# Optimization experiments

Hardware: AMD Instinct MI355X
Metric: run time of the kernel (lower is better)

## Reference

```python
import jax, jax.numpy as jnp
import numpy as np

D = 2048
H = 16
HD = D // H  # 128


def setup_inputs() -> dict:
    key = jax.random.key(0)
    k1, k2, k3 = jax.random.split(key, 3)
    x = jax.random.normal(k1, (2, 2048, D), dtype=jnp.float32)
    # nn.Linear(d, 3d, bias=False): weight [3d, d]; y = x @ W.T
    w_qkv = jax.random.normal(k2, (3 * D, D), dtype=jnp.float32) * (1.0 / np.sqrt(D))
    w_o = jax.random.normal(k3, (D, D), dtype=jnp.float32) * (1.0 / np.sqrt(D))
    return {"x": x, "w_qkv": w_qkv, "w_o": w_o}


def reference(x, w_qkv, w_o):
    B, T, _ = x.shape
    qkv = jnp.einsum('btd,ed->bte', x, w_qkv)  # [B,T,3D]
    q, k, v = jnp.split(qkv, 3, axis=-1)
    # [B,T,D] -> [B,H,T,hd]
    q = q.reshape(B, T, H, HD).transpose(0, 2, 1, 3)
    k = k.reshape(B, T, H, HD).transpose(0, 2, 1, 3)
    v = v.reshape(B, T, H, HD).transpose(0, 2, 1, 3)
    att = jnp.einsum('bhtd,bhsd->bhts', q, k) / np.sqrt(HD).astype(np.float32)
    att = jax.nn.softmax(att, axis=-1)
    y = jnp.einsum('bhts,bhsd->bhtd', att, v)
    y = y.transpose(0, 2, 1, 3).reshape(B, T, D)
    return jnp.einsum('btd,ed->bte', y, w_o)
```

## Files before the change

### kernel.cpp

```cpp
#include <hip/hip_runtime.h>
#include <hip/hip_bf16.h>
#include <math.h>

typedef __bf16 bf16_t;
typedef __attribute__((ext_vector_type(8))) __bf16 bx8;
typedef __attribute__((ext_vector_type(4))) __bf16 bx4;
typedef __attribute__((ext_vector_type(4))) float fx4;

#define DEV __device__ __forceinline__

DEV void async_copy16(void* lds, const void* g) {
    __builtin_amdgcn_global_load_lds(
        (const __attribute__((address_space(1))) unsigned int*)g,
        (__attribute__((address_space(3))) unsigned int*)lds, 16, 0, 0);
}

__global__ void __launch_bounds__(256) cvt_bf16(const float* __restrict__ in,
                                                bf16_t* __restrict__ out, int n) {
    int i = (blockIdx.x * 256 + threadIdx.x) * 4;
    if (i + 3 < n) {
        float4 v = *(const float4*)(in + i);
        bx4 o = { (__bf16)v.x, (__bf16)v.y, (__bf16)v.z, (__bf16)v.w };
        *(bx4*)(out + i) = o;
    }
}

template <bool BF16_OUT>
__global__ void __launch_bounds__(256, 2) gemm_bt(const bf16_t* __restrict__ A,
                                                  const bf16_t* __restrict__ B,
                                                  void* __restrict__ C,
                                                  int M, int N, int K) {
    __shared__ bf16_t As[2 * 4096];
    __shared__ bf16_t Bs[2 * 4096];
    const int tid = threadIdx.x;
    const int w = tid >> 6, lane = tid & 63;
    const int ln = lane & 15, quad = lane >> 4;
    const int m0 = blockIdx.y * 128, n0 = blockIdx.x * 128;
    const int wm = (w >> 1) * 64, wn = (w & 1) * 64;

    fx4 acc[4][4];
#pragma unroll
    for (int i = 0; i < 4; ++i)
#pragma unroll
        for (int j = 0; j < 4; ++j) acc[i][j] = (fx4){0.f, 0.f, 0.f, 0.f};

    for (int k0 = 0; k0 < K; k0 += 64) {
#pragma unroll
        for (int call = 0; call < 4; ++call) {
            int c = w * 256 + call * 64 + lane;
            int p = c >> 9, row = (c >> 2) & 127, piece = c & 3;
            async_copy16(As + (size_t)(w * 256 + call * 64) * 8,
                         A + (size_t)(m0 + row) * K + k0 + p * 32 + piece * 8);
            async_copy16(Bs + (size_t)(w * 256 + call * 64) * 8,
                         B + (size_t)(n0 + row) * K + k0 + p * 32 + piece * 8);
        }
        __syncthreads();

#pragma unroll
        for (int kk = 0; kk < 2; ++kk) {
            bx8 af[4], bf[4];
#pragma unroll
            for (int i = 0; i < 4; ++i)
                af[i] = *(const bx8*)(As + (size_t)kk * 4096 + (wm + i * 16 + ln) * 32 + quad * 8);
#pragma unroll
            for (int j = 0; j < 4; ++j)
                bf[j] = *(const bx8*)(Bs + (size_t)kk * 4096 + (wn + j * 16 + ln) * 32 + quad * 8);
#pragma unroll
            for (int i = 0; i < 4; ++i)
#pragma unroll
                for (int j = 0; j < 4; ++j)
                    acc[i][j] = __builtin_amdgcn_mfma_f32_16x16x32_bf16(af[i], bf[j], acc[i][j], 0, 0, 0);
        }
        __syncthreads();
    }

#pragma unroll
    for (int i = 0; i < 4; ++i) {
        int mrow = m0 + wm + i * 16 + quad * 4;
#pragma unroll
        for (int j = 0; j < 4; ++j) {
            int ncol = n0 + wn + j * 16 + ln;
#pragma unroll
            for (int r = 0; r < 4; ++r) {
                if (BF16_OUT)
                    ((bf16_t*)C)[(size_t)(mrow + r) * N + ncol] = (__bf16)acc[i][j][r];
                else
                    ((float*)C)[(size_t)(mrow + r) * N + ncol] = acc[i][j][r];
            }
        }
    }
}

__global__ void __launch_bounds__(256) vtrans(const bf16_t* __restrict__ qkv,
                                              bf16_t* __restrict__ vt) {
    __shared__ bf16_t tile[64][65];
    const int tid = threadIdx.x;
    const int bh = blockIdx.z;
    const int b = bh >> 4, h = bh & 15;
    const int t0 = blockIdx.x * 64, hd0 = blockIdx.y * 64;
    const bf16_t* src = qkv + (size_t)(b * 2048 + t0) * 6144 + 4096 + h * 128 + hd0;
    const int rr = tid >> 6, cc = tid & 63;
#pragma unroll
    for (int i = 0; i < 16; ++i)
        tile[rr + i * 4][cc] = src[(size_t)(rr + i * 4) * 6144 + cc];
    __syncthreads();
    bf16_t* dst = vt + ((size_t)bh * 128 + hd0) * 2048 + t0;
#pragma unroll
    for (int i = 0; i < 16; ++i)
        dst[(size_t)(rr + i * 4) * 2048 + cc] = tile[cc][rr + i * 4];
}

__global__ void __launch_bounds__(256, 2) attn(const bf16_t* __restrict__ qkv,
                                               const bf16_t* __restrict__ vt,
                                               bf16_t* __restrict__ y) {
    __shared__ bf16_t Ks[128 * 128];
    __shared__ bf16_t Vs[128 * 128];
    __shared__ bf16_t Ps[4 * 1024];
    const int tid = threadIdx.x;
    const int w = tid >> 6, lane = tid & 63;
    const int ln = lane & 15, quad = lane >> 4;
    const int lin = blockIdx.x;
    const int slot = lin >> 3;
    const int bh = (lin & 7) + ((slot >> 4) << 3);
    const int qt = slot & 15;
    const int b = bh >> 4, h = bh & 15;
    const float CEXP = 0.08838834764831845f * 1.44269504088896340f;

    const bf16_t* Qb = qkv + (size_t)(b * 2048 + qt * 128) * 6144 + h * 128;
    const bf16_t* Kb = qkv + (size_t)(b * 2048) * 6144 + 2048 + h * 128;
    const bf16_t* Vb = vt + (size_t)bh * 128 * 2048;

    bx8 qf[2][4];
#pragma unroll
    for (int i = 0; i < 2; ++i)
#pragma unroll
        for (int kk = 0; kk < 4; ++kk)
            qf[i][kk] = *(const bx8*)(Qb + (size_t)(w * 32 + i * 16 + ln) * 6144 + kk * 32 + quad * 8);

    const __bf16 one = (__bf16)1.0f;
    const bx8 ones = { one, one, one, one, one, one, one, one };

    fx4 o[2][8];
#pragma unroll
    for (int i = 0; i < 2; ++i)
#pragma unroll
        for (int j = 0; j < 8; ++j) o[i][j] = (fx4){0.f, 0.f, 0.f, 0.f};
    fx4 lsum[2];
#pragma unroll
    for (int i = 0; i < 2; ++i) lsum[i] = (fx4){0.f, 0.f, 0.f, 0.f};

    bf16_t* Pw = Ps + (size_t)w * 1024;

    for (int kt = 0; kt < 16; ++kt) {
#pragma unroll
        for (int call = 0; call < 8; ++call) {
            int cp = call * 64 + lane;
            int row = cp >> 2, piece = cp & 3;
            async_copy16(Ks + (size_t)w * 4096 + call * 512,
                         Kb + (size_t)(kt * 128 + row) * 6144 + w * 32 + piece * 8);
            async_copy16(Vs + (size_t)w * 4096 + call * 512,
                         Vb + (size_t)row * 2048 + kt * 128 + w * 32 + piece * 8);
        }
        __syncthreads();

#pragma unroll
        for (int q = 0; q < 4; ++q) {
            fx4 s[2][2];
#pragma unroll
            for (int i = 0; i < 2; ++i)
#pragma unroll
                for (int jj = 0; jj < 2; ++jj) s[i][jj] = (fx4){0.f, 0.f, 0.f, 0.f};
#pragma unroll
            for (int kk = 0; kk < 4; ++kk) {
                bx8 kf0 = *(const bx8*)(Ks + (size_t)kk * 4096 + ((2 * q) * 16 + ln) * 32 + quad * 8);
                bx8 kf1 = *(const bx8*)(Ks + (size_t)kk * 4096 + ((2 * q + 1) * 16 + ln) * 32 + quad * 8);
#pragma unroll
                for (int i = 0; i < 2; ++i) {
                    s[i][0] = __builtin_amdgcn_mfma_f32_16x16x32_bf16(qf[i][kk], kf0, s[i][0], 0, 0, 0);
                    s[i][1] = __builtin_amdgcn_mfma_f32_16x16x32_bf16(qf[i][kk], kf1, s[i][1], 0, 0, 0);
                }
            }

#pragma unroll
            for (int i = 0; i < 2; ++i)
#pragma unroll
                for (int jj = 0; jj < 2; ++jj)
#pragma unroll
                    for (int r = 0; r < 4; ++r) {
                        float p = exp2f(s[i][jj][r] * CEXP);
                        int prow = i * 16 + quad * 4 + r;
                        Pw[prow * 32 + ((jj * 16 + ln) ^ (quad << 3))] = (__bf16)p;
                    }

#pragma unroll
            for (int i = 0; i < 2; ++i) {
                bx8 pf = *(const bx8*)(Pw + (size_t)(i * 16 + ln) * 32 +
                                       ((quad ^ ((ln >> 2) & 3)) << 3));
#pragma unroll
                for (int j = 0; j < 8; ++j) {
                    bx8 vf = *(const bx8*)(Vs + (size_t)q * 4096 + (j * 16 + ln) * 32 + quad * 8);
                    o[i][j] = __builtin_amdgcn_mfma_f32_16x16x32_bf16(pf, vf, o[i][j], 0, 0, 0);
                }
                lsum[i] = __builtin_amdgcn_mfma_f32_16x16x32_bf16(pf, ones, lsum[i], 0, 0, 0);
            }
        }
        __syncthreads();
    }

#pragma unroll
    for (int i = 0; i < 2; ++i)
#pragma unroll
        for (int r = 0; r < 4; ++r) {
            float rl = 1.0f / lsum[i][r];
#pragma unroll
            for (int j = 0; j < 8; ++j) {
                int t = qt * 128 + w * 32 + i * 16 + quad * 4 + r;
                int col = h * 128 + j * 16 + ln;
                y[(size_t)(b * 2048 + t) * 2048 + col] = (__bf16)(o[i][j][r] * rl);
            }
        }
}

extern "C" void kernel_launch(void* const* d_in, const int* in_sizes, int n_in,
                              void* d_out, int out_size, void* d_ws, size_t ws_size,
                              hipStream_t stream) {
    const float* x    = (const float*)d_in[0];
    const float* wqkv = (const float*)d_in[1];
    const float* wo   = (const float*)d_in[2];
    float* out = (float*)d_out;
    char* ws = (char*)d_ws;

    bf16_t* Xb  = (bf16_t*)(ws);
    bf16_t* Wqb = (bf16_t*)(ws + (size_t)(16u << 20));
    bf16_t* Wob = (bf16_t*)(ws + (size_t)(40u << 20));
    bf16_t* QKV = (bf16_t*)(ws + (size_t)(48u << 20));
    bf16_t* VT  = (bf16_t*)(ws + (size_t)(96u << 20));
    bf16_t* Y   = Xb;

    cvt_bf16<<<8388608 / 1024, 256, 0, stream>>>(x, Xb, 8388608);
    cvt_bf16<<<12582912 / 1024, 256, 0, stream>>>(wqkv, Wqb, 12582912);
    cvt_bf16<<<4194304 / 1024, 256, 0, stream>>>(wo, Wob, 4194304);

    gemm_bt<true><<<dim3(48, 32), 256, 0, stream>>>(Xb, Wqb, QKV, 4096, 6144, 2048);
    vtrans<<<dim3(32, 2, 32), 256, 0, stream>>>(QKV, VT);
    attn<<<dim3(512), 256, 0, stream>>>(QKV, VT, Y);
    gemm_bt<false><<<dim3(16, 32), 256, 0, stream>>>(Y, Wob, out, 4096, 2048, 2048);
}
```

Before: 382.6 us.

## Keep attention probabilities in registers via transposed S and packed V layout

The score MFMA is computed transposed (K as A operand), so each lane's accumulator already forms the A-operand fragment for a 16x16x16 PV MFMA. This removes the per-wave LDS round trip for P and its shared buffer. V is repacked by a new vpack kernel into 4-token interleaved groups that match the bx4 B-operand layout, replacing the tiled transpose. The softmax scale times log2e is folded into the Q columns in the QKV GEMM epilogue, which drops a multiply per exp. The cost is twice as many, smaller MFMAs for PV, plus rounding Q after scaling, which slightly changes numerics.

```diff
diff --git a/kernel.cpp b/kernel.cpp
--- a/kernel.cpp
+++ b/kernel.cpp
@@ -5,6 +5,7 @@
 typedef __bf16 bf16_t;
 typedef __attribute__((ext_vector_type(8))) __bf16 bx8;
 typedef __attribute__((ext_vector_type(4))) __bf16 bx4;
+typedef __attribute__((ext_vector_type(4))) short sx4;
 typedef __attribute__((ext_vector_type(4))) float fx4;
 
 #define DEV __device__ __forceinline__
@@ -13,6 +14,18 @@
     __builtin_amdgcn_global_load_lds(
         (const __attribute__((address_space(1))) unsigned int*)g,
         (__attribute__((address_space(3))) unsigned int*)lds, 16, 0, 0);
+}
+
+DEV fx4 mfma16(bx4 a, bx4 b, fx4 c) {
+#if __has_builtin(__builtin_amdgcn_mfma_f32_16x16x16bf16_1k)
+    return __builtin_amdgcn_mfma_f32_16x16x16bf16_1k(
+        __builtin_bit_cast(sx4, a), __builtin_bit_cast(sx4, b), c, 0, 0, 0);
+#elif __has_builtin(__builtin_amdgcn_mfma_f32_16x16x16_bf16)
+    return __builtin_amdgcn_mfma_f32_16x16x16_bf16(a, b, c, 0, 0, 0);
+#else
+    asm("v_mfma_f32_16x16x16_bf16 %0, %1, %2, %0" : "+v"(c) : "v"(a), "v"(b));
+    return c;
+#endif
 }
 
 __global__ void __launch_bounds__(256) cvt_bf16(const float* __restrict__ in,
@@ -29,7 +42,7 @@
 __global__ void __launch_bounds__(256, 2) gemm_bt(const bf16_t* __restrict__ A,
                                                   const bf16_t* __restrict__ B,
                                                   void* __restrict__ C,
-                                                  int M, int N, int K) {
+                                                  int M, int N, int K, float scale0) {
     __shared__ bf16_t As[2 * 4096];
     __shared__ bf16_t Bs[2 * 4096];
     const int tid = threadIdx.x;
@@ -37,6 +50,7 @@
     const int ln = lane & 15, quad = lane >> 4;
     const int m0 = blockIdx.y * 128, n0 = blockIdx.x * 128;
     const int wm = (w >> 1) * 64, wn = (w & 1) * 64;
+    const float scale = (n0 < 2048) ? scale0 : 1.0f;
 
     fx4 acc[4][4];
 #pragma unroll
@@ -83,7 +97,7 @@
 #pragma unroll
             for (int r = 0; r < 4; ++r) {
                 if (BF16_OUT)
-                    ((bf16_t*)C)[(size_t)(mrow + r) * N + ncol] = (__bf16)acc[i][j][r];
+                    ((bf16_t*)C)[(size_t)(mrow + r) * N + ncol] = (__bf16)(acc[i][j][r] * scale);
                 else
                     ((float*)C)[(size_t)(mrow + r) * N + ncol] = acc[i][j][r];
             }
@@ -91,31 +105,32 @@
     }
 }
 
-__global__ void __launch_bounds__(256) vtrans(const bf16_t* __restrict__ qkv,
-                                              bf16_t* __restrict__ vt) {
-    __shared__ bf16_t tile[64][65];
-    const int tid = threadIdx.x;
-    const int bh = blockIdx.z;
-    const int b = bh >> 4, h = bh & 15;
-    const int t0 = blockIdx.x * 64, hd0 = blockIdx.y * 64;
-    const bf16_t* src = qkv + (size_t)(b * 2048 + t0) * 6144 + 4096 + h * 128 + hd0;
-    const int rr = tid >> 6, cc = tid & 63;
-#pragma unroll
-    for (int i = 0; i < 16; ++i)
-        tile[rr + i * 4][cc] = src[(size_t)(rr + i * 4) * 6144 + cc];
-    __syncthreads();
-    bf16_t* dst = vt + ((size_t)bh * 128 + hd0) * 2048 + t0;
-#pragma unroll
-    for (int i = 0; i < 16; ++i)
-        dst[(size_t)(rr + i * 4) * 2048 + cc] = tile[cc][rr + i * 4];
+__global__ void __launch_bounds__(256) vpack(const bf16_t* __restrict__ qkv,
+                                             bf16_t* __restrict__ vp) {
+    int g = blockIdx.x * 256 + threadIdx.x;
+    int bh = g >> 15;
+    int rem = g & 32767;
+    int q4 = rem >> 6;
+    int c  = rem & 63;
+    int b = bh >> 4, h = bh & 15;
+    const bf16_t* src = qkv + (size_t)(b * 2048 + q4 * 4) * 6144 + 4096 + h * 128 + c * 2;
+    unsigned u0 = *(const unsigned*)(src);
+    unsigned u1 = *(const unsigned*)(src + 6144);
+    unsigned u2 = *(const unsigned*)(src + 12288);
+    unsigned u3 = *(const unsigned*)(src + 18432);
+    uint4 outv;
+    outv.x = (u0 & 0xffffu) | (u1 << 16);
+    outv.y = (u2 & 0xffffu) | (u3 << 16);
+    outv.z = (u0 >> 16) | (u1 & 0xffff0000u);
+    outv.w = (u2 >> 16) | (u3 & 0xffff0000u);
+    *(uint4*)(vp + (size_t)g * 8) = outv;
 }
 
 __global__ void __launch_bounds__(256, 2) attn(const bf16_t* __restrict__ qkv,
-                                               const bf16_t* __restrict__ vt,
+                                               const bf16_t* __restrict__ vp,
                                                bf16_t* __restrict__ y) {
     __shared__ bf16_t Ks[128 * 128];
-    __shared__ bf16_t Vs[128 * 128];
-    __shared__ bf16_t Ps[4 * 1024];
+    __shared__ bf16_t Vs[16384];
     const int tid = threadIdx.x;
     const int w = tid >> 6, lane = tid & 63;
     const int ln = lane & 15, quad = lane >> 4;
@@ -124,11 +139,10 @@
     const int bh = (lin & 7) + ((slot >> 4) << 3);
     const int qt = slot & 15;
     const int b = bh >> 4, h = bh & 15;
-    const float CEXP = 0.08838834764831845f * 1.44269504088896340f;
 
     const bf16_t* Qb = qkv + (size_t)(b * 2048 + qt * 128) * 6144 + h * 128;
     const bf16_t* Kb = qkv + (size_t)(b * 2048) * 6144 + 2048 + h * 128;
-    const bf16_t* Vb = vt + (size_t)bh * 128 * 2048;
+    const bf16_t* VPb = vp + (size_t)bh * 262144;
 
     bx8 qf[2][4];
 #pragma unroll
@@ -138,7 +152,7 @@
             qf[i][kk] = *(const bx8*)(Qb + (size_t)(w * 32 + i * 16 + ln) * 6144 + kk * 32 + quad * 8);
 
     const __bf16 one = (__bf16)1.0f;
-    const bx8 ones = { one, one, one, one, one, one, one, one };
+    const bx4 ones4 = { one, one, one, one };
 
     fx4 o[2][8];
 #pragma unroll
@@ -148,8 +162,6 @@
     fx4 lsum[2];
 #pragma unroll
     for (int i = 0; i < 2; ++i) lsum[i] = (fx4){0.f, 0.f, 0.f, 0.f};
-
-    bf16_t* Pw = Ps + (size_t)w * 1024;
 
     for (int kt = 0; kt < 16; ++kt) {
 #pragma unroll
@@ -159,49 +171,52 @@
             async_copy16(Ks + (size_t)w * 4096 + call * 512,
                          Kb + (size_t)(kt * 128 + row) * 6144 + w * 32 + piece * 8);
             async_copy16(Vs + (size_t)w * 4096 + call * 512,
-                         Vb + (size_t)row * 2048 + kt * 128 + w * 32 + piece * 8);
+                         VPb + (size_t)kt * 16384 + (w * 8 + call) * 512 + lane * 8);
         }
         __syncthreads();
 
 #pragma unroll
         for (int q = 0; q < 4; ++q) {
-            fx4 s[2][2];
+            fx4 st[2][2];
 #pragma unroll
             for (int i = 0; i < 2; ++i)
 #pragma unroll
-                for (int jj = 0; jj < 2; ++jj) s[i][jj] = (fx4){0.f, 0.f, 0.f, 0.f};
+                for (int jj = 0; jj < 2; ++jj) st[i][jj] = (fx4){0.f, 0.f, 0.f, 0.f};
 #pragma unroll
             for (int kk = 0; kk < 4; ++kk) {
                 bx8 kf0 = *(const bx8*)(Ks + (size_t)kk * 4096 + ((2 * q) * 16 + ln) * 32 + quad * 8);
                 bx8 kf1 = *(const bx8*)(Ks + (size_t)kk * 4096 + ((2 * q + 1) * 16 + ln) * 32 + quad * 8);
 #pragma unroll
                 for (int i = 0; i < 2; ++i) {
-                    s[i][0] = __builtin_amdgcn_mfma_f32_16x16x32_bf16(qf[i][kk], kf0, s[i][0], 0, 0, 0);
-                    s[i][1] = __builtin_amdgcn_mfma_f32_16x16x32_bf16(qf[i][kk], kf1, s[i][1], 0, 0, 0);
+                    st[i][0] = __builtin_amdgcn_mfma_f32_16x16x32_bf16(kf0, qf[i][kk], st[i][0], 0, 0, 0);
+                    st[i][1] = __builtin_amdgcn_mfma_f32_16x16x32_bf16(kf1, qf[i][kk], st[i][1], 0, 0, 0);
                 }
             }
 
+            bx4 pa[2][2];
 #pragma unroll
             for (int i = 0; i < 2; ++i)
 #pragma unroll
-                for (int jj = 0; jj < 2; ++jj)
-#pragma unroll
-                    for (int r = 0; r < 4; ++r) {
-                        float p = exp2f(s[i][jj][r] * CEXP);
-                        int prow = i * 16 + quad * 4 + r;
-                        Pw[prow * 32 + ((jj * 16 + ln) ^ (quad << 3))] = (__bf16)p;
-                    }
-
-#pragma unroll
-            for (int i = 0; i < 2; ++i) {
-                bx8 pf = *(const bx8*)(Pw + (size_t)(i * 16 + ln) * 32 +
-                                       ((quad ^ ((ln >> 2) & 3)) << 3));
-#pragma unroll
-                for (int j = 0; j < 8; ++j) {
-                    bx8 vf = *(const bx8*)(Vs + (size_t)q * 4096 + (j * 16 + ln) * 32 + quad * 8);
-                    o[i][j] = __builtin_amdgcn_mfma_f32_16x16x32_bf16(pf, vf, o[i][j], 0, 0, 0);
+                for (int jj = 0; jj < 2; ++jj) {
+                    bx4 t = { (__bf16)exp2f(st[i][jj][0]), (__bf16)exp2f(st[i][jj][1]),
+                              (__bf16)exp2f(st[i][jj][2]), (__bf16)exp2f(st[i][jj][3]) };
+                    pa[i][jj] = t;
                 }
-                lsum[i] = __builtin_amdgcn_mfma_f32_16x16x32_bf16(pf, ones, lsum[i], 0, 0, 0);
+
+#pragma unroll
+            for (int jj = 0; jj < 2; ++jj) {
+                const int kt8 = 2 * q + jj;
+                bx4 vf[8];
+#pragma unroll
+                for (int j = 0; j < 8; ++j)
+                    vf[j] = *(const bx4*)(Vs + (size_t)(kt8 * 4 + quad) * 512 + (j * 16 + ln) * 4);
+#pragma unroll
+                for (int i = 0; i < 2; ++i) {
+#pragma unroll
+                    for (int j = 0; j < 8; ++j)
+                        o[i][j] = mfma16(pa[i][jj], vf[j], o[i][j]);
+                    lsum[i] = mfma16(pa[i][jj], ones4, lsum[i]);
+                }
             }
         }
         __syncthreads();
@@ -229,20 +244,21 @@
     const float* wo   = (const float*)d_in[2];
     float* out = (float*)d_out;
     char* ws = (char*)d_ws;
+    const float CEXP = 0.08838834764831845f * 1.44269504088896340f;
 
     bf16_t* Xb  = (bf16_t*)(ws);
     bf16_t* Wqb = (bf16_t*)(ws + (size_t)(16u << 20));
     bf16_t* Wob = (bf16_t*)(ws + (size_t)(40u << 20));
     bf16_t* QKV = (bf16_t*)(ws + (size_t)(48u << 20));
-    bf16_t* VT  = (bf16_t*)(ws + (size_t)(96u << 20));
+    bf16_t* VP  = (bf16_t*)(ws + (size_t)(96u << 20));
     bf16_t* Y   = Xb;
 
     cvt_bf16<<<8388608 / 1024, 256, 0, stream>>>(x, Xb, 8388608);
     cvt_bf16<<<12582912 / 1024, 256, 0, stream>>>(wqkv, Wqb, 12582912);
     cvt_bf16<<<4194304 / 1024, 256, 0, stream>>>(wo, Wob, 4194304);
 
-    gemm_bt<true><<<dim3(48, 32), 256, 0, stream>>>(Xb, Wqb, QKV, 4096, 6144, 2048);
-    vtrans<<<dim3(32, 2, 32), 256, 0, stream>>>(QKV, VT);
-    attn<<<dim3(512), 256, 0, stream>>>(QKV, VT, Y);
-    gemm_bt<false><<<dim3(16, 32), 256, 0, stream>>>(Y, Wob, out, 4096, 2048, 2048);
-}
+    gemm_bt<true><<<dim3(48, 32), 256, 0, stream>>>(Xb, Wqb, QKV, 4096, 6144, 2048, CEXP);
+    vpack<<<4096, 256, 0, stream>>>(QKV, VP);
+    attn<<<dim3(512), 256, 0, stream>>>(QKV, VP, Y);
+    gemm_bt<false><<<dim3(16, 32), 256, 0, stream>>>(Y, Wob, out, 4096, 2048, 2048, 1.0f);
+}
```

New measurement: 387.3 us. About the same (+1.2%).
